# Performance work log

Measured on AMD Instinct MI355X. Metric: run time of the kernel, lower is better.

Reference implementation:

```python
import jax, jax.numpy as jnp
import numpy as np

D_EMBED = 1024
N_HEADS = 16
D_HEAD = D_EMBED // N_HEADS
B, S1, S2 = 2, 2048, 2048


def setup_inputs() -> dict:
    key = jax.random.key(0)
    ks = jax.random.split(key, 10)
    sc = 1.0 / np.sqrt(D_EMBED)
    return {
        "x1": jax.random.normal(ks[0], (B, S1, D_EMBED), dtype=jnp.float32),
        "x2": jax.random.normal(ks[1], (B, S2, D_EMBED), dtype=jnp.float32),
        # torch nn.Linear convention: weight [out, in], y = x @ W.T + b
        "Wq": jax.random.normal(ks[2], (D_EMBED, D_EMBED), dtype=jnp.float32) * sc,
        "bq": jax.random.normal(ks[3], (D_EMBED,), dtype=jnp.float32) * sc,
        "Wk": jax.random.normal(ks[4], (D_EMBED, D_EMBED), dtype=jnp.float32) * sc,
        "bk": jax.random.normal(ks[5], (D_EMBED,), dtype=jnp.float32) * sc,
        "Wv": jax.random.normal(ks[6], (D_EMBED, D_EMBED), dtype=jnp.float32) * sc,
        "bv": jax.random.normal(ks[7], (D_EMBED,), dtype=jnp.float32) * sc,
        "Wo": jax.random.normal(ks[8], (D_EMBED, D_EMBED), dtype=jnp.float32) * sc,
        "bo": jax.random.normal(ks[9], (D_EMBED,), dtype=jnp.float32) * sc,
    }


def reference(x1, x2, Wq, bq, Wk, bk, Wv, bv, Wo, bo):
    b, s1, _ = x1.shape
    s2 = x2.shape[1]
    # projections, split heads: [b, h, s, d_head]
    Q = (x1 @ Wq.T + bq).reshape(b, s1, N_HEADS, D_HEAD).transpose(0, 2, 1, 3)
    K = (x2 @ Wk.T + bk).reshape(b, s2, N_HEADS, D_HEAD).transpose(0, 2, 1, 3)
    V = (x2 @ Wv.T + bv).reshape(b, s2, N_HEADS, D_HEAD).transpose(0, 2, 1, 3)
    scores = jnp.einsum("bhqd,bhkd->bhqk", Q, K) / jnp.sqrt(jnp.float32(D_HEAD))
    attn_weights = jax.nn.softmax(scores, axis=-1)
    attn_out = jnp.einsum("bhqk,bhkd->bhqd", attn_weights, V)
    attn_out = attn_out.transpose(0, 2, 1, 3).reshape(b, s1, D_EMBED)
    output = attn_out @ Wo.T + bo
    return output, attn_weights
```

## Files before the change

kernel.cpp:

```cpp
#include <hip/hip_runtime.h>
#include <stdint.h>

#define D_EMBEDC 1024
#define N_HEADSC 16
#define D_HEADC  64
#define BATCHC   2
#define S1C      2048
#define S2C      2048

typedef __attribute__((ext_vector_type(8))) short short8;
typedef __attribute__((ext_vector_type(4))) float floatx4;

__device__ __forceinline__ ushort f2bf(float x) {
    uint32_t u = __float_as_uint(x);
    uint32_t r = (u + 0x7fffu + ((u >> 16) & 1u)) >> 16;
    return (ushort)r;
}

__device__ __forceinline__ void glds16(const void* g, void* l) {
    __builtin_amdgcn_global_load_lds(
        (const __attribute__((address_space(1))) void*)g,
        (__attribute__((address_space(3))) void*)l, 16, 0, 0);
}

__global__ __launch_bounds__(256)
void cast_f32_bf16(const float4* __restrict__ in, ushort4* __restrict__ out)
{
    const int i = blockIdx.x * 256 + threadIdx.x;
    float4 v = in[i];
    ushort4 o;
    o.x = f2bf(v.x); o.y = f2bf(v.y); o.z = f2bf(v.z); o.w = f2bf(v.w);
    out[i] = o;
}

__global__ __launch_bounds__(256)
void qkv_mfma(const ushort* __restrict__ x1b, const ushort* __restrict__ x2b,
              const ushort* __restrict__ Wqb, const ushort* __restrict__ Wkb,
              const ushort* __restrict__ Wvb,
              const float* __restrict__ bq, const float* __restrict__ bk,
              const float* __restrict__ bv,
              ushort* __restrict__ Qb, ushort* __restrict__ Kb,
              ushort* __restrict__ Vtb)
{
    __shared__ __align__(16) ushort As[128 * 32];
    __shared__ __align__(16) ushort Bs[128 * 32];

    const int which = blockIdx.z;
    const ushort* A = (which == 0) ? x1b : x2b;
    const ushort* W = (which == 0) ? Wqb : (which == 1) ? Wkb : Wvb;
    const float* bias = (which == 0) ? bq : (which == 1) ? bk : bv;

    const int tid = threadIdx.x;
    const int lane = tid & 63;
    const int wave = tid >> 6;
    const int m0 = blockIdx.x * 128;
    const int n0 = blockIdx.y * 128;
    const int wm = (wave & 1) * 64;
    const int wn = (wave >> 1) * 64;
    const int K = 1024;

    floatx4 zero = {0.f, 0.f, 0.f, 0.f};
    floatx4 acc[4][4];
#pragma unroll
    for (int i = 0; i < 4; ++i)
#pragma unroll
        for (int j = 0; j < 4; ++j) acc[i][j] = zero;

    for (int k0 = 0; k0 < K; k0 += 32) {
#pragma unroll
        for (int i = 0; i < 2; ++i) {
            const int f = i * 256 + tid;
            const int r = f >> 2, kc = (f & 3) * 8;
            glds16(A + (size_t)(m0 + r) * K + k0 + kc, &As[f * 8]);
            glds16(W + (size_t)(n0 + r) * K + k0 + kc, &Bs[f * 8]);
        }
        __syncthreads();
        short8 a[4], b[4];
#pragma unroll
        for (int t = 0; t < 4; ++t) {
            a[t] = *(const short8*)&As[(wm + t * 16 + (lane & 15)) * 32 + (lane >> 4) * 8];
            b[t] = *(const short8*)&Bs[(wn + t * 16 + (lane & 15)) * 32 + (lane >> 4) * 8];
        }
#pragma unroll
        for (int im = 0; im < 4; ++im)
#pragma unroll
            for (int in = 0; in < 4; ++in)
                acc[im][in] = __builtin_amdgcn_mfma_f32_16x16x32_bf16(a[im], b[in], acc[im][in], 0, 0, 0);
        __syncthreads();
    }

#pragma unroll
    for (int im = 0; im < 4; ++im) {
#pragma unroll
        for (int in = 0; in < 4; ++in) {
            const int mbase = m0 + wm + im * 16 + ((lane >> 4) << 2);
            const int n = n0 + wn + in * 16 + (lane & 15);
            const int h = n >> 6, d = n & 63;
            const float bv_ = bias[n];
            if (which < 2) {
                ushort* outp = (which == 0) ? Qb : Kb;
#pragma unroll
                for (int r = 0; r < 4; ++r) {
                    const int m = mbase + r;
                    const int bb = m >> 11, s = m & 2047;
                    outp[((((size_t)(bb * 16 + h)) * 2048 + s) << 6) + d] =
                        f2bf(acc[im][in][r] + bv_);
                }
            } else {
                const int m = mbase;
                const int bb = m >> 11, s = m & 2047;
                const size_t base = (((size_t)(bb * 16 + h) * 64 + d) << 11) + s;
                ushort4 pk;
                pk.x = f2bf(acc[im][in][0] + bv_);
                pk.y = f2bf(acc[im][in][1] + bv_);
                pk.z = f2bf(acc[im][in][2] + bv_);
                pk.w = f2bf(acc[im][in][3] + bv_);
                *(ushort4*)&Vtb[base] = pk;
            }
        }
    }
}

__global__ __launch_bounds__(256, 2)
void fused_attn(const ushort* __restrict__ Qb, const ushort* __restrict__ Kb,
                const ushort* __restrict__ Vtb, float* __restrict__ P,
                ushort* __restrict__ Ab)
{
    __shared__ __align__(16) ushort Ks[2][128][32];
    __shared__ __align__(16) ushort Vs[4][64][32];
    __shared__ __align__(16) ushort Ps[128][136];

    const int bid = blockIdx.x;
    const int logical = (bid & 7) * 64 + (bid >> 3);
    const int z = logical >> 4;
    const int m0 = (logical & 15) * 128;

    const ushort* Qz = Qb + (size_t)z * S1C * D_HEADC;
    const ushort* Kz = Kb + (size_t)z * S2C * D_HEADC;
    const ushort* Vz = Vtb + (size_t)z * D_HEADC * S2C;
    float* Pz = P + (size_t)z * S1C * S2C;

    const int tid = threadIdx.x;
    const int lane = tid & 63;
    const int wave = tid >> 6;
    const int wm = (wave & 1) * 64;
    const int wn = (wave >> 1) * 64;
    const int lg = lane >> 4;
    const int ll = lane & 15;

    short8 a_q[4][2];
    {
#pragma unroll
        for (int i = 0; i < 4; ++i) {
            const int f = i * 256 + tid;
            const int dc = f >> 9, row = (f >> 2) & 127, q = f & 3;
            glds16(Qz + (size_t)(m0 + row) * D_HEADC + dc * 32 + q * 8,
                   &Ks[dc][row][q * 8]);
        }
        __syncthreads();
#pragma unroll
        for (int im = 0; im < 4; ++im)
#pragma unroll
            for (int dc = 0; dc < 2; ++dc)
                a_q[im][dc] = *(const short8*)&Ks[dc][wm + im * 16 + ll][lg * 8];
        __syncthreads();
    }

    floatx4 zero = {0.f, 0.f, 0.f, 0.f};

    float psum[4][4];
#pragma unroll
    for (int im = 0; im < 4; ++im)
#pragma unroll
        for (int r = 0; r < 4; ++r) psum[im][r] = 0.f;

    for (int k0 = 0; k0 < S2C; k0 += 128) {
#pragma unroll
        for (int i = 0; i < 4; ++i) {
            const int f = i * 256 + tid;
            const int dc = f >> 9, row = (f >> 2) & 127, q = f & 3;
            glds16(Kz + (size_t)(k0 + row) * D_HEADC + dc * 32 + q * 8,
                   &Ks[dc][row][q * 8]);
        }
        __syncthreads();

        floatx4 acc[4][4];
#pragma unroll
        for (int i = 0; i < 4; ++i)
#pragma unroll
            for (int j = 0; j < 4; ++j) acc[i][j] = zero;
#pragma unroll
        for (int dc = 0; dc < 2; ++dc) {
            short8 b[4];
#pragma unroll
            for (int in = 0; in < 4; ++in)
                b[in] = *(const short8*)&Ks[dc][wn + in * 16 + ll][lg * 8];
#pragma unroll
            for (int im = 0; im < 4; ++im)
#pragma unroll
                for (int in = 0; in < 4; ++in)
                    acc[im][in] = __builtin_amdgcn_mfma_f32_16x16x32_bf16(a_q[im][dc], b[in], acc[im][in], 0, 0, 0);
        }
        __syncthreads();

#pragma unroll
        for (int im = 0; im < 4; ++im)
#pragma unroll
            for (int r = 0; r < 4; ++r)
                psum[im][r] += __expf(acc[im][0][r] * 0.125f) + __expf(acc[im][1][r] * 0.125f)
                             + __expf(acc[im][2][r] * 0.125f) + __expf(acc[im][3][r] * 0.125f);
    }

    float* rowsum = (float*)&Ps[0][0];
#pragma unroll
    for (int im = 0; im < 4; ++im)
#pragma unroll
        for (int r = 0; r < 4; ++r) {
            float s = psum[im][r];
            s += __shfl_xor(s, 1); s += __shfl_xor(s, 2);
            s += __shfl_xor(s, 4); s += __shfl_xor(s, 8);
            psum[im][r] = s;
        }
    if (ll == 0) {
#pragma unroll
        for (int im = 0; im < 4; ++im)
#pragma unroll
            for (int r = 0; r < 4; ++r)
                rowsum[(wave >> 1) * 128 + wm + im * 16 + lg * 4 + r] = psum[im][r];
    }
    __syncthreads();
    float inv_l[4][4];
#pragma unroll
    for (int im = 0; im < 4; ++im)
#pragma unroll
        for (int r = 0; r < 4; ++r) {
            const int row = wm + im * 16 + lg * 4 + r;
            inv_l[im][r] = 1.0f / (rowsum[row] + rowsum[128 + row]);
        }
    __syncthreads();

    floatx4 acc_o[2][4];
#pragma unroll
    for (int i = 0; i < 2; ++i)
#pragma unroll
        for (int j = 0; j < 4; ++j) acc_o[i][j] = zero;
    const int wm2 = wave * 32;

    for (int k0 = 0; k0 < S2C; k0 += 128) {
#pragma unroll
        for (int i = 0; i < 4; ++i) {
            const int f = i * 256 + tid;
            const int dc = f >> 9, row = (f >> 2) & 127, q = f & 3;
            glds16(Kz + (size_t)(k0 + row) * D_HEADC + dc * 32 + q * 8,
                   &Ks[dc][row][q * 8]);
        }
#pragma unroll
        for (int i = 0; i < 4; ++i) {
            const int f = i * 256 + tid;
            const int kc = f >> 8, d = (f >> 2) & 63, q = f & 3;
            glds16(Vz + (size_t)d * S2C + k0 + kc * 32 + q * 8,
                   &Vs[kc][d][q * 8]);
        }
        __syncthreads();

        floatx4 acc[4][4];
#pragma unroll
        for (int i = 0; i < 4; ++i)
#pragma unroll
            for (int j = 0; j < 4; ++j) acc[i][j] = zero;
#pragma unroll
        for (int dc = 0; dc < 2; ++dc) {
            short8 b[4];
#pragma unroll
            for (int in = 0; in < 4; ++in)
                b[in] = *(const short8*)&Ks[dc][wn + in * 16 + ll][lg * 8];
#pragma unroll
            for (int im = 0; im < 4; ++im)
#pragma unroll
                for (int in = 0; in < 4; ++in)
                    acc[im][in] = __builtin_amdgcn_mfma_f32_16x16x32_bf16(a_q[im][dc], b[in], acc[im][in], 0, 0, 0);
        }

#pragma unroll
        for (int im = 0; im < 4; ++im) {
            const int rowb = wm + im * 16 + lg * 4;
#pragma unroll
            for (int in = 0; in < 4; ++in) {
                const int col = wn + in * 16 + ll;
#pragma unroll
                for (int r = 0; r < 4; ++r) {
                    const float pn = __expf(acc[im][in][r] * 0.125f) * inv_l[im][r];
                    Pz[(size_t)(m0 + rowb + r) * S2C + k0 + col] = pn;
                    Ps[rowb + r][col] = f2bf(pn);
                }
            }
        }
        __syncthreads();

#pragma unroll
        for (int kc = 0; kc < 4; ++kc) {
            short8 a[2], b[4];
#pragma unroll
            for (int t = 0; t < 2; ++t)
                a[t] = *(const short8*)&Ps[wm2 + t * 16 + ll][kc * 32 + lg * 8];
#pragma unroll
            for (int t = 0; t < 4; ++t)
                b[t] = *(const short8*)&Vs[kc][t * 16 + ll][lg * 8];
#pragma unroll
            for (int im = 0; im < 2; ++im)
#pragma unroll
                for (int in = 0; in < 4; ++in)
                    acc_o[im][in] = __builtin_amdgcn_mfma_f32_16x16x32_bf16(a[im], b[in], acc_o[im][in], 0, 0, 0);
        }
        __syncthreads();
    }

    const int h = z & 15, bb = z >> 4;
#pragma unroll
    for (int im = 0; im < 2; ++im)
#pragma unroll
        for (int in = 0; in < 4; ++in) {
            const int mbase = m0 + wm2 + im * 16 + lg * 4;
            const int col = h * 64 + in * 16 + ll;
#pragma unroll
            for (int r = 0; r < 4; ++r)
                Ab[(size_t)(bb * 2048 + mbase + r) * 1024 + col] = f2bf(acc_o[im][in][r]);
        }
}

__global__ __launch_bounds__(256)
void gemm_out_mfma(const ushort* __restrict__ A, const ushort* __restrict__ W,
                   const float* __restrict__ bias, float* __restrict__ out)
{
    __shared__ __align__(16) ushort As[128 * 32];
    __shared__ __align__(16) ushort Bs[128 * 32];

    const int tid = threadIdx.x;
    const int lane = tid & 63;
    const int wave = tid >> 6;
    const int m0 = blockIdx.x * 128;
    const int n0 = blockIdx.y * 128;
    const int wm = (wave & 1) * 64;
    const int wn = (wave >> 1) * 64;
    const int K = 1024, N = 1024;

    floatx4 zero = {0.f, 0.f, 0.f, 0.f};
    floatx4 acc[4][4];
#pragma unroll
    for (int i = 0; i < 4; ++i)
#pragma unroll
        for (int j = 0; j < 4; ++j) acc[i][j] = zero;

    for (int k0 = 0; k0 < K; k0 += 32) {
#pragma unroll
        for (int i = 0; i < 2; ++i) {
            const int f = i * 256 + tid;
            const int r = f >> 2, kc = (f & 3) * 8;
            glds16(A + (size_t)(m0 + r) * K + k0 + kc, &As[f * 8]);
            glds16(W + (size_t)(n0 + r) * K + k0 + kc, &Bs[f * 8]);
        }
        __syncthreads();
        short8 a[4], b[4];
#pragma unroll
        for (int t = 0; t < 4; ++t) {
            a[t] = *(const short8*)&As[(wm + t * 16 + (lane & 15)) * 32 + (lane >> 4) * 8];
            b[t] = *(const short8*)&Bs[(wn + t * 16 + (lane & 15)) * 32 + (lane >> 4) * 8];
        }
#pragma unroll
        for (int im = 0; im < 4; ++im)
#pragma unroll
            for (int in = 0; in < 4; ++in)
                acc[im][in] = __builtin_amdgcn_mfma_f32_16x16x32_bf16(a[im], b[in], acc[im][in], 0, 0, 0);
        __syncthreads();
    }

#pragma unroll
    for (int im = 0; im < 4; ++im)
#pragma unroll
        for (int in = 0; in < 4; ++in) {
            const int mbase = m0 + wm + im * 16 + ((lane >> 4) << 2);
            const int n = n0 + wn + in * 16 + (lane & 15);
            const float bv_ = bias[n];
#pragma unroll
            for (int r = 0; r < 4; ++r)
                out[(size_t)(mbase + r) * N + n] = acc[im][in][r] + bv_;
        }
}

extern "C" void kernel_launch(void* const* d_in, const int* in_sizes, int n_in,
                              void* d_out, int out_size, void* d_ws, size_t ws_size,
                              hipStream_t stream)
{
    const float* x1 = (const float*)d_in[0];
    const float* x2 = (const float*)d_in[1];
    const float* Wq = (const float*)d_in[2];
    const float* bq = (const float*)d_in[3];
    const float* Wk = (const float*)d_in[4];
    const float* bk = (const float*)d_in[5];
    const float* Wv = (const float*)d_in[6];
    const float* bv = (const float*)d_in[7];
    const float* Wo = (const float*)d_in[8];
    const float* bo = (const float*)d_in[9];

    float* out   = (float*)d_out;
    float* attnw = out + (size_t)BATCHC * S1C * D_EMBEDC;

    const size_t XSZ = (size_t)BATCHC * S1C * D_EMBEDC;
    const size_t WSZ = (size_t)D_EMBEDC * D_EMBEDC;
    ushort* w = (ushort*)d_ws;
    ushort* x1b = w;            w += XSZ;
    ushort* x2b = w;            w += XSZ;
    ushort* Wqb = w;            w += WSZ;
    ushort* Wkb = w;            w += WSZ;
    ushort* Wvb = w;            w += WSZ;
    ushort* Wob = w;            w += WSZ;
    ushort* Qb  = w;            w += XSZ;
    ushort* Kb  = w;            w += XSZ;
    ushort* Vtb = w;            w += XSZ;
    ushort* Ab  = w;            w += XSZ;

    const dim3 blk(256);

    cast_f32_bf16<<<dim3(XSZ / 1024), blk, 0, stream>>>((const float4*)x1, (ushort4*)x1b);
    cast_f32_bf16<<<dim3(XSZ / 1024), blk, 0, stream>>>((const float4*)x2, (ushort4*)x2b);
    cast_f32_bf16<<<dim3(WSZ / 1024), blk, 0, stream>>>((const float4*)Wq, (ushort4*)Wqb);
    cast_f32_bf16<<<dim3(WSZ / 1024), blk, 0, stream>>>((const float4*)Wk, (ushort4*)Wkb);
    cast_f32_bf16<<<dim3(WSZ / 1024), blk, 0, stream>>>((const float4*)Wv, (ushort4*)Wvb);
    cast_f32_bf16<<<dim3(WSZ / 1024), blk, 0, stream>>>((const float4*)Wo, (ushort4*)Wob);

    qkv_mfma<<<dim3(32, 8, 3), blk, 0, stream>>>(x1b, x2b, Wqb, Wkb, Wvb,
                                                 bq, bk, bv, Qb, Kb, Vtb);

    fused_attn<<<dim3(512), blk, 0, stream>>>(Qb, Kb, Vtb, attnw, Ab);

    gemm_out_mfma<<<dim3(32, 8), blk, 0, stream>>>(Ab, Wob, bo, out);
}
```

Baseline: 715.1 us.

## Load K/V/Q fragments directly from global, drop LDS staging, fuse cast kernels

The attention kernel now reads Q, K and V MFMA operands straight from global memory into registers instead of staging them through LDS with global_load_lds. This removes several barriers per iteration and frees shared memory. The remaining barriers use a custom macro that waits only on LDS counters. Separately, the six cast launches are merged into one kernel. The cost is redundant global/L2 traffic, since each wave refetches K tiles other waves also use, plus uncoalesced 16-byte row loads and more load latency that is no longer overlapped.

```diff
diff --git a/kernel.cpp b/kernel.cpp
--- a/kernel.cpp
+++ b/kernel.cpp
@@ -23,14 +23,31 @@
         (__attribute__((address_space(3))) void*)l, 16, 0, 0);
 }
 
+#define BARX() do { asm volatile("s_waitcnt lgkmcnt(0)" ::: "memory"); \
+                    __builtin_amdgcn_s_barrier();                      \
+                    __builtin_amdgcn_sched_barrier(0); } while (0)
+
 __global__ __launch_bounds__(256)
-void cast_f32_bf16(const float4* __restrict__ in, ushort4* __restrict__ out)
+void cast_all(const float4* __restrict__ x1, const float4* __restrict__ x2,
+              const float4* __restrict__ Wq, const float4* __restrict__ Wk,
+              const float4* __restrict__ Wv, const float4* __restrict__ Wo,
+              ushort4* __restrict__ x1b, ushort4* __restrict__ x2b,
+              ushort4* __restrict__ Wqb, ushort4* __restrict__ Wkb,
+              ushort4* __restrict__ Wvb, ushort4* __restrict__ Wob)
 {
-    const int i = blockIdx.x * 256 + threadIdx.x;
-    float4 v = in[i];
+    const int b = blockIdx.x;
+    const float4* src; ushort4* dst; int off;
+    if (b < 4096)       { src = x1; dst = x1b; off = b; }
+    else if (b < 8192)  { src = x2; dst = x2b; off = b - 4096; }
+    else if (b < 9216)  { src = Wq; dst = Wqb; off = b - 8192; }
+    else if (b < 10240) { src = Wk; dst = Wkb; off = b - 9216; }
+    else if (b < 11264) { src = Wv; dst = Wvb; off = b - 10240; }
+    else                { src = Wo; dst = Wob; off = b - 11264; }
+    const int i = off * 256 + threadIdx.x;
+    float4 v = src[i];
     ushort4 o;
     o.x = f2bf(v.x); o.y = f2bf(v.y); o.z = f2bf(v.z); o.w = f2bf(v.w);
-    out[i] = o;
+    dst[i] = o;
 }
 
 __global__ __launch_bounds__(256)
@@ -126,8 +143,6 @@
                 const ushort* __restrict__ Vtb, float* __restrict__ P,
                 ushort* __restrict__ Ab)
 {
-    __shared__ __align__(16) ushort Ks[2][128][32];
-    __shared__ __align__(16) ushort Vs[4][64][32];
     __shared__ __align__(16) ushort Ps[128][136];
 
     const int bid = blockIdx.x;
@@ -149,22 +164,11 @@
     const int ll = lane & 15;
 
     short8 a_q[4][2];
-    {
-#pragma unroll
-        for (int i = 0; i < 4; ++i) {
-            const int f = i * 256 + tid;
-            const int dc = f >> 9, row = (f >> 2) & 127, q = f & 3;
-            glds16(Qz + (size_t)(m0 + row) * D_HEADC + dc * 32 + q * 8,
-                   &Ks[dc][row][q * 8]);
-        }
-        __syncthreads();
-#pragma unroll
-        for (int im = 0; im < 4; ++im)
-#pragma unroll
-            for (int dc = 0; dc < 2; ++dc)
-                a_q[im][dc] = *(const short8*)&Ks[dc][wm + im * 16 + ll][lg * 8];
-        __syncthreads();
-    }
+#pragma unroll
+    for (int im = 0; im < 4; ++im)
+#pragma unroll
+        for (int dc = 0; dc < 2; ++dc)
+            a_q[im][dc] = *(const short8*)&Qz[(size_t)(m0 + wm + im * 16 + ll) * D_HEADC + dc * 32 + lg * 8];
 
     floatx4 zero = {0.f, 0.f, 0.f, 0.f};
 
@@ -175,14 +179,12 @@
         for (int r = 0; r < 4; ++r) psum[im][r] = 0.f;
 
     for (int k0 = 0; k0 < S2C; k0 += 128) {
-#pragma unroll
-        for (int i = 0; i < 4; ++i) {
-            const int f = i * 256 + tid;
-            const int dc = f >> 9, row = (f >> 2) & 127, q = f & 3;
-            glds16(Kz + (size_t)(k0 + row) * D_HEADC + dc * 32 + q * 8,
-                   &Ks[dc][row][q * 8]);
-        }
-        __syncthreads();
+        short8 b[2][4];
+#pragma unroll
+        for (int dc = 0; dc < 2; ++dc)
+#pragma unroll
+            for (int in = 0; in < 4; ++in)
+                b[dc][in] = *(const short8*)&Kz[(size_t)(k0 + wn + in * 16 + ll) * D_HEADC + dc * 32 + lg * 8];
 
         floatx4 acc[4][4];
 #pragma unroll
@@ -190,18 +192,12 @@
 #pragma unroll
             for (int j = 0; j < 4; ++j) acc[i][j] = zero;
 #pragma unroll
-        for (int dc = 0; dc < 2; ++dc) {
-            short8 b[4];
-#pragma unroll
-            for (int in = 0; in < 4; ++in)
-                b[in] = *(const short8*)&Ks[dc][wn + in * 16 + ll][lg * 8];
+        for (int dc = 0; dc < 2; ++dc)
 #pragma unroll
             for (int im = 0; im < 4; ++im)
 #pragma unroll
                 for (int in = 0; in < 4; ++in)
-                    acc[im][in] = __builtin_amdgcn_mfma_f32_16x16x32_bf16(a_q[im][dc], b[in], acc[im][in], 0, 0, 0);
-        }
-        __syncthreads();
+                    acc[im][in] = __builtin_amdgcn_mfma_f32_16x16x32_bf16(a_q[im][dc], b[dc][in], acc[im][in], 0, 0, 0);
 
 #pragma unroll
         for (int im = 0; im < 4; ++im)
@@ -247,21 +243,12 @@
     const int wm2 = wave * 32;
 
     for (int k0 = 0; k0 < S2C; k0 += 128) {
-#pragma unroll
-        for (int i = 0; i < 4; ++i) {
-            const int f = i * 256 + tid;
-            const int dc = f >> 9, row = (f >> 2) & 127, q = f & 3;
-            glds16(Kz + (size_t)(k0 + row) * D_HEADC + dc * 32 + q * 8,
-                   &Ks[dc][row][q * 8]);
-        }
-#pragma unroll
-        for (int i = 0; i < 4; ++i) {
-            const int f = i * 256 + tid;
-            const int kc = f >> 8, d = (f >> 2) & 63, q = f & 3;
-            glds16(Vz + (size_t)d * S2C + k0 + kc * 32 + q * 8,
-                   &Vs[kc][d][q * 8]);
-        }
-        __syncthreads();
+        short8 b[2][4];
+#pragma unroll
+        for (int dc = 0; dc < 2; ++dc)
+#pragma unroll
+            for (int in = 0; in < 4; ++in)
+                b[dc][in] = *(const short8*)&Kz[(size_t)(k0 + wn + in * 16 + ll) * D_HEADC + dc * 32 + lg * 8];
 
         floatx4 acc[4][4];
 #pragma unroll
@@ -269,17 +256,12 @@
 #pragma unroll
             for (int j = 0; j < 4; ++j) acc[i][j] = zero;
 #pragma unroll
-        for (int dc = 0; dc < 2; ++dc) {
-            short8 b[4];
-#pragma unroll
-            for (int in = 0; in < 4; ++in)
-                b[in] = *(const short8*)&Ks[dc][wn + in * 16 + ll][lg * 8];
+        for (int dc = 0; dc < 2; ++dc)
 #pragma unroll
             for (int im = 0; im < 4; ++im)
 #pragma unroll
                 for (int in = 0; in < 4; ++in)
-                    acc[im][in] = __builtin_amdgcn_mfma_f32_16x16x32_bf16(a_q[im][dc], b[in], acc[im][in], 0, 0, 0);
-        }
+                    acc[im][in] = __builtin_amdgcn_mfma_f32_16x16x32_bf16(a_q[im][dc], b[dc][in], acc[im][in], 0, 0, 0);
 
 #pragma unroll
         for (int im = 0; im < 4; ++im) {
@@ -295,24 +277,24 @@
                 }
             }
         }
-        __syncthreads();
+        BARX();
 
 #pragma unroll
         for (int kc = 0; kc < 4; ++kc) {
-            short8 a[2], b[4];
+            short8 a[2], bv[4];
 #pragma unroll
             for (int t = 0; t < 2; ++t)
                 a[t] = *(const short8*)&Ps[wm2 + t * 16 + ll][kc * 32 + lg * 8];
 #pragma unroll
             for (int t = 0; t < 4; ++t)
-                b[t] = *(const short8*)&Vs[kc][t * 16 + ll][lg * 8];
+                bv[t] = *(const short8*)&Vz[(size_t)(t * 16 + ll) * S2C + k0 + kc * 32 + lg * 8];
 #pragma unroll
             for (int im = 0; im < 2; ++im)
 #pragma unroll
                 for (int in = 0; in < 4; ++in)
-                    acc_o[im][in] = __builtin_amdgcn_mfma_f32_16x16x32_bf16(a[im], b[in], acc_o[im][in], 0, 0, 0);
-        }
-        __syncthreads();
+                    acc_o[im][in] = __builtin_amdgcn_mfma_f32_16x16x32_bf16(a[im], bv[in], acc_o[im][in], 0, 0, 0);
+        }
+        BARX();
     }
 
     const int h = z & 15, bb = z >> 4;
@@ -421,12 +403,11 @@
 
     const dim3 blk(256);
 
-    cast_f32_bf16<<<dim3(XSZ / 1024), blk, 0, stream>>>((const float4*)x1, (ushort4*)x1b);
-    cast_f32_bf16<<<dim3(XSZ / 1024), blk, 0, stream>>>((const float4*)x2, (ushort4*)x2b);
-    cast_f32_bf16<<<dim3(WSZ / 1024), blk, 0, stream>>>((const float4*)Wq, (ushort4*)Wqb);
-    cast_f32_bf16<<<dim3(WSZ / 1024), blk, 0, stream>>>((const float4*)Wk, (ushort4*)Wkb);
-    cast_f32_bf16<<<dim3(WSZ / 1024), blk, 0, stream>>>((const float4*)Wv, (ushort4*)Wvb);
-    cast_f32_bf16<<<dim3(WSZ / 1024), blk, 0, stream>>>((const float4*)Wo, (ushort4*)Wob);
+    cast_all<<<dim3(12288), blk, 0, stream>>>(
+        (const float4*)x1, (const float4*)x2, (const float4*)Wq, (const float4*)Wk,
+        (const float4*)Wv, (const float4*)Wo,
+        (ushort4*)x1b, (ushort4*)x2b, (ushort4*)Wqb, (ushort4*)Wkb,
+        (ushort4*)Wvb, (ushort4*)Wob);
 
     qkv_mfma<<<dim3(32, 8, 3), blk, 0, stream>>>(x1b, x2b, Wqb, Wkb, Wvb,
                                                  bq, bk, bv, Qb, Kb, Vtb);
```

New measurement: 765.3 us. +7.0%, slower.
